# Performance work log

Hardware: AMD Instinct MI355X
Metric: run time of the kernel (lower is better)

Reference implementation:

```python
import jax, jax.numpy as jnp
import numpy as np

N = 50000; E = 800000; H = 4; C = 64; FEAT = 128; EDIM = 16; G = 256
NEG_SLOPE = 0.2; BN_EPS = 1e-5


def _gat_layer(x, src, dst, W, a_src, a_dst, bias, gamma, beta, alpha_edge=None):
    # GATConv (concat=True, PyG math), then BatchNorm1d (batch stats) + ReLU.
    h = (x @ W).reshape(N, H, C)                       # [N,H,C]
    alpha = (h * a_src).sum(-1)[src] + (h * a_dst).sum(-1)[dst]   # [Etot,H]
    if alpha_edge is not None:
        alpha = alpha + alpha_edge
    alpha = jax.nn.leaky_relu(alpha, NEG_SLOPE)
    amax = jax.ops.segment_max(alpha, dst, num_segments=N)        # edge softmax over dst
    ea = jnp.exp(alpha - amax[dst])
    denom = jax.ops.segment_sum(ea, dst, num_segments=N)
    coef = ea / (denom[dst] + 1e-16)
    out = jax.ops.segment_sum(coef[:, :, None] * h[src], dst, num_segments=N)
    out = out.reshape(N, H * C) + bias
    mu = out.mean(0)
    var = out.var(0)
    out = (out - mu) / jnp.sqrt(var + BN_EPS) * gamma + beta
    return jax.nn.relu(out)


def setup_inputs() -> dict:
    key = jax.random.key(0)
    ks = jax.random.split(key, 32)
    s = 0.05
    inp = {
        "x": jax.random.normal(ks[0], (N, FEAT), jnp.float32),
        "edge_index": jax.random.randint(ks[1], (2, E), 0, N),
        "edge_attr": jax.random.normal(ks[2], (E, EDIM), jnp.float32),
        "batch": jnp.sort(jax.random.randint(ks[3], (N,), 0, G)),
    }
    in_dims = [FEAT, H * C, H * C]
    for i in range(3):
        k = 4 + 7 * i
        inp[f"W{i}"] = jax.random.normal(ks[k], (in_dims[i], H * C), jnp.float32) * s
        inp[f"att_src{i}"] = jax.random.normal(ks[k + 1], (H, C), jnp.float32) * s
        inp[f"att_dst{i}"] = jax.random.normal(ks[k + 2], (H, C), jnp.float32) * s
        inp[f"bias{i}"] = jnp.zeros((H * C,), jnp.float32)
        inp[f"gamma{i}"] = jnp.ones((H * C,), jnp.float32)
        inp[f"beta{i}"] = jnp.zeros((H * C,), jnp.float32)
    inp["We0"] = jax.random.normal(ks[28], (EDIM, H * C), jnp.float32) * s
    inp["att_e0"] = jax.random.normal(ks[29], (H, C), jnp.float32) * s
    return inp


def reference(x, edge_index, edge_attr, batch,
              W0, att_src0, att_dst0, bias0, gamma0, beta0,
              W1, att_src1, att_dst1, bias1, gamma1, beta1,
              W2, att_src2, att_dst2, bias2, gamma2, beta2,
              We0, att_e0):
    # PyG GATConv adds self-loops; edge_attr for self-loops filled with mean.
    loops = jnp.arange(N)
    src = jnp.concatenate([edge_index[0], loops])
    dst = jnp.concatenate([edge_index[1], loops])
    ea_sl = jnp.concatenate([edge_attr, jnp.broadcast_to(edge_attr.mean(0), (N, EDIM))], 0)
    e = (ea_sl @ We0).reshape(E + N, H, C)
    alpha_e = (e * att_e0).sum(-1)                     # [Etot,H]
    x = _gat_layer(x, src, dst, W0, att_src0, att_dst0, bias0, gamma0, beta0, alpha_e)
    x = _gat_layer(x, src, dst, W1, att_src1, att_dst1, bias1, gamma1, beta1)
    x = _gat_layer(x, src, dst, W2, att_src2, att_dst2, bias2, gamma2, beta2)
    # global_mean_pool
    counts = jax.ops.segment_sum(jnp.ones((N,), x.dtype), batch, num_segments=G)
    sums = jax.ops.segment_sum(x, batch, num_segments=G)
    return sums / jnp.clip(counts, 1.0)[:, None]
```

## Files before the change

kernel.cpp:

```cpp
#include <hip/hip_runtime.h>
#include <math.h>

#define NN 50000
#define NE 800000
#define ET 850000
#define HCC 256
#define GG 256
#define CAP 64
#define NB 16

constexpr size_t NHC    = (size_t)NN * HCC;
constexpr size_t O_H    = 0;
constexpr size_t O_AGG  = O_H + NHC / 2;
constexpr size_t O_REC  = O_AGG + NHC / 2;
constexpr size_t O_BT0  = O_REC + (size_t)NN * CAP * 4;
constexpr size_t O_BT1  = O_BT0 + 16384;
constexpr size_t O_BT2  = O_BT1 + 32768;
constexpr size_t O_AS   = O_BT2 + 32768;
constexpr size_t O_AD   = O_AS + (size_t)NN * 4;
constexpr size_t O_M    = O_AD + (size_t)NN * 4;
constexpr size_t O_ZERO = O_M + 64;
constexpr size_t O_DEG  = O_ZERO;
constexpr size_t O_SLS  = O_DEG + NN;
constexpr size_t O_PART = O_SLS + 4;
constexpr size_t O_END  = O_PART + 3 * NB * 512;
constexpr size_t ZWORDS = O_END - O_ZERO;
constexpr int    ZBLK   = (int)((ZWORDS / 4 + 255) / 256);

typedef __attribute__((ext_vector_type(8))) short bf16x8;
typedef __attribute__((ext_vector_type(4))) float f32x4;

__device__ inline unsigned short f2bf(float f) {
    unsigned int u = __float_as_uint(f);
    unsigned int r = (u + 0x7fffu + ((u >> 16) & 1u)) >> 16;
    return (unsigned short)r;
}
__device__ inline float b2f(unsigned short u) {
    return __uint_as_float(((unsigned int)u) << 16);
}
__device__ inline float bflo(unsigned int u) { return __uint_as_float(u << 16); }
__device__ inline float bfhi(unsigned int u) { return __uint_as_float(u & 0xffff0000u); }

__global__ void prep_kernel(const float* __restrict__ W0, const float* __restrict__ W1,
                            const float* __restrict__ W2,
                            const float* __restrict__ We0, const float* __restrict__ att_e0,
                            unsigned short* __restrict__ Bt0,
                            unsigned short* __restrict__ Bt1,
                            unsigned short* __restrict__ Bt2,
                            float* __restrict__ M, float* __restrict__ zbase) {
    int b = blockIdx.x;
    if (b >= 641) {
        size_t idx = ((size_t)(b - 641) * 256 + threadIdx.x) * 4;
        if (idx < ZWORDS)
            *(float4*)(zbase + idx) = make_float4(0.f, 0.f, 0.f, 0.f);
        return;
    }
    if (b == 640) {
        int t = threadIdx.x;
        if (t < 64) {
            int k = t >> 2, hh = t & 3;
            float s = 0.f;
            for (int c = 0; c < 64; ++c)
                s += We0[k * 256 + hh * 64 + c] * att_e0[hh * 64 + c];
            M[k * 4 + hh] = s;
        }
        return;
    }
    const float* W; unsigned short* Bt; int K, base;
    if (b < 128)      { W = W0; Bt = Bt0; K = 128; base = 0; }
    else if (b < 384) { W = W1; Bt = Bt1; K = 256; base = 128; }
    else              { W = W2; Bt = Bt2; K = 256; base = 384; }
    int idx = (b - base) * 256 + threadIdx.x;
    int n = idx & 255, k = idx >> 8;
    Bt[(size_t)n * K + k] = f2bf(W[(size_t)k * 256 + n]);
}

__global__ void csr_kernel(const int* __restrict__ srcA, const int* __restrict__ dstA,
                           const float* __restrict__ ea, const float* __restrict__ M,
                           int* __restrict__ deg, uint4* __restrict__ rec,
                           float* __restrict__ slsum) {
    int t0 = blockIdx.x * 2048 + threadIdx.x;
    float a0 = 0.f, a1 = 0.f, a2 = 0.f, a3 = 0.f;
    #pragma unroll
    for (int q = 0; q < 8; ++q) {
        int e = t0 + q * 256;
        if (e < ET) {
            bool real = (e < NE);
            int d = real ? dstA[e] : (e - NE);
            int s = real ? srcA[e] : (e - NE);
            int p = atomicAdd(&deg[d], 1);
            if (p > CAP - 1) p = CAP - 1;
            int slot = d * CAP + p;
            uint4 r;
            r.z = (unsigned)s;
            if (real) {
                r.w = 0u;
                const float4* pp = (const float4*)(ea + (size_t)e * 16);
                float4 va = pp[0], vb = pp[1], vc = pp[2], vd = pp[3];
                float v[16] = {va.x, va.y, va.z, va.w, vb.x, vb.y, vb.z, vb.w,
                               vc.x, vc.y, vc.z, vc.w, vd.x, vd.y, vd.z, vd.w};
                float o0 = 0.f, o1 = 0.f, o2 = 0.f, o3 = 0.f;
                #pragma unroll
                for (int k = 0; k < 16; ++k) {
                    float4 m4 = *(const float4*)(M + k * 4);
                    o0 = fmaf(v[k], m4.x, o0);
                    o1 = fmaf(v[k], m4.y, o1);
                    o2 = fmaf(v[k], m4.z, o2);
                    o3 = fmaf(v[k], m4.w, o3);
                }
                r.x = ((unsigned)f2bf(o1) << 16) | (unsigned)f2bf(o0);
                r.y = ((unsigned)f2bf(o3) << 16) | (unsigned)f2bf(o2);
                a0 += o0; a1 += o1; a2 += o2; a3 += o3;
            } else {
                r.x = 0u; r.y = 0u; r.w = 1u;
            }
            rec[slot] = r;
        }
    }
    #pragma unroll
    for (int off = 32; off; off >>= 1) {
        a0 += __shfl_xor(a0, off);
        a1 += __shfl_xor(a1, off);
        a2 += __shfl_xor(a2, off);
        a3 += __shfl_xor(a3, off);
    }
    __shared__ float part[4][4];
    int wave = threadIdx.x >> 6, lane = threadIdx.x & 63;
    if (lane == 0) {
        part[wave][0] = a0; part[wave][1] = a1;
        part[wave][2] = a2; part[wave][3] = a3;
    }
    __syncthreads();
    if (threadIdx.x < 4)
        atomicAdd(&slsum[threadIdx.x],
                  part[0][threadIdx.x] + part[1][threadIdx.x] +
                  part[2][threadIdx.x] + part[3][threadIdx.x]);
}

template <int K, bool NORM>
__global__ __launch_bounds__(256) void gemm_fused(const float* __restrict__ Af,
                                                  const unsigned short* __restrict__ Ab,
                                                  const unsigned short* __restrict__ Bt,
                                                  const float* __restrict__ part,
                                                  const float* __restrict__ gamma,
                                                  const float* __restrict__ beta,
                                                  const float* __restrict__ att_src,
                                                  const float* __restrict__ att_dst,
                                                  unsigned short* __restrict__ Hout,
                                                  float* __restrict__ asA,
                                                  float* __restrict__ adA, int M) {
    __shared__ unsigned short As[64][40];
    __shared__ unsigned short Bs[256][40];
    __shared__ float kvs[256], cvs[256];
    int tid = threadIdx.x;
    int wave = tid >> 6, lane = tid & 63;
    int quad = lane >> 4, l16 = lane & 15;
    int row0 = blockIdx.x * 64;
    f32x4 acc[4][4] = {};

    if (NORM) {
        int ch = tid;
        float s = 0.f, s2 = 0.f;
        #pragma unroll
        for (int b = 0; b < NB; ++b) {
            s  += part[b * 512 + ch];
            s2 += part[b * 512 + 256 + ch];
        }
        const float invN = 1.0f / (float)NN;
        float mr = s * invN;
        float var = s2 * invN - mr * mr;
        float k = gamma[ch] * rsqrtf(var + 1e-5f);
        kvs[ch] = k;
        cvs[ch] = beta[ch] - mr * k;
        __syncthreads();
    }

    for (int k0 = 0; k0 < K; k0 += 32) {
        {
            int row = tid >> 2, seg = tid & 3;
            ushort4 o0 = make_ushort4(0, 0, 0, 0), o1 = o0;
            if (row0 + row < M) {
                float u[8];
                if (NORM) {
                    uint4 raw = *(const uint4*)(Ab + (size_t)(row0 + row) * K + k0 + seg * 8);
                    u[0] = bflo(raw.x); u[1] = bfhi(raw.x);
                    u[2] = bflo(raw.y); u[3] = bfhi(raw.y);
                    u[4] = bflo(raw.z); u[5] = bfhi(raw.z);
                    u[6] = bflo(raw.w); u[7] = bfhi(raw.w);
                    int cb = k0 + seg * 8;
                    #pragma unroll
                    for (int q = 0; q < 8; ++q)
                        u[q] = fmaxf(fmaf(u[q], kvs[cb + q], cvs[cb + q]), 0.f);
                } else {
                    const float* ap = Af + (size_t)(row0 + row) * K + k0 + seg * 8;
                    float4 f1 = *(const float4*)ap;
                    float4 f2 = *(const float4*)(ap + 4);
                    u[0] = f1.x; u[1] = f1.y; u[2] = f1.z; u[3] = f1.w;
                    u[4] = f2.x; u[5] = f2.y; u[6] = f2.z; u[7] = f2.w;
                }
                o0 = make_ushort4(f2bf(u[0]), f2bf(u[1]), f2bf(u[2]), f2bf(u[3]));
                o1 = make_ushort4(f2bf(u[4]), f2bf(u[5]), f2bf(u[6]), f2bf(u[7]));
            }
            *(ushort4*)&As[row][seg * 8] = o0;
            *(ushort4*)&As[row][seg * 8 + 4] = o1;
        }
        {
            const uint4* src = (const uint4*)(Bt + (size_t)tid * K + k0);
            uint4 b0 = src[0], b1 = src[1], b2 = src[2], b3 = src[3];
            uint4* dst = (uint4*)&Bs[tid][0];
            dst[0] = b0; dst[1] = b1; dst[2] = b2; dst[3] = b3;
        }
        __syncthreads();
        bf16x8 a_frag[4], b_frag[4];
        #pragma unroll
        for (int mi = 0; mi < 4; ++mi)
            a_frag[mi] = *(const bf16x8*)&As[mi * 16 + l16][quad * 8];
        #pragma unroll
        for (int ni = 0; ni < 4; ++ni)
            b_frag[ni] = *(const bf16x8*)&Bs[wave * 64 + ni * 16 + l16][quad * 8];
        #pragma unroll
        for (int mi = 0; mi < 4; ++mi)
            #pragma unroll
            for (int ni = 0; ni < 4; ++ni)
                acc[mi][ni] = __builtin_amdgcn_mfma_f32_16x16x32_bf16(
                    a_frag[mi], b_frag[ni], acc[mi][ni], 0, 0, 0);
        __syncthreads();
    }

    #pragma unroll
    for (int mi = 0; mi < 4; ++mi) {
        #pragma unroll
        for (int reg = 0; reg < 4; ++reg) {
            int r = row0 + mi * 16 + quad * 4 + reg;
            if (r < M) {
                #pragma unroll
                for (int ni = 0; ni < 4; ++ni) {
                    int c = wave * 64 + ni * 16 + l16;
                    Hout[(size_t)r * HCC + c] = f2bf(acc[mi][ni][reg]);
                }
            }
        }
    }
    float asc[4], adc_[4];
    #pragma unroll
    for (int ni = 0; ni < 4; ++ni) {
        asc[ni] = att_src[wave * 64 + ni * 16 + l16];
        adc_[ni] = att_dst[wave * 64 + ni * 16 + l16];
    }
    #pragma unroll
    for (int mi = 0; mi < 4; ++mi) {
        #pragma unroll
        for (int reg = 0; reg < 4; ++reg) {
            float s1 = acc[mi][0][reg] * asc[0] + acc[mi][1][reg] * asc[1] +
                       acc[mi][2][reg] * asc[2] + acc[mi][3][reg] * asc[3];
            float d1 = acc[mi][0][reg] * adc_[0] + acc[mi][1][reg] * adc_[1] +
                       acc[mi][2][reg] * adc_[2] + acc[mi][3][reg] * adc_[3];
            #pragma unroll
            for (int off = 1; off < 16; off <<= 1) {
                s1 += __shfl_xor(s1, off);
                d1 += __shfl_xor(d1, off);
            }
            int r = row0 + mi * 16 + quad * 4 + reg;
            if (l16 == 0 && r < M) {
                asA[(size_t)r * 4 + wave] = s1;
                adA[(size_t)r * 4 + wave] = d1;
            }
        }
    }
}

template <bool HAS_AE>
__global__ __launch_bounds__(512) void agg_kernel(const unsigned short* __restrict__ Hm,
                                                  const float* __restrict__ asA,
                                                  const float* __restrict__ adA,
                                                  const uint4* __restrict__ rec,
                                                  const int* __restrict__ degA,
                                                  const float* __restrict__ slsum,
                                                  unsigned short* __restrict__ outA,
                                                  float* __restrict__ part) {
    __shared__ float wlds[8][260];
    __shared__ float slds[2][8][256];
    int wave = threadIdx.x >> 6, lane = threadIdx.x & 63;
    int n = blockIdx.x * 8 + wave;
    int head = lane >> 4;
    int st = n * CAP;
    int d = degA[n];
    if (d > CAP) d = CAP;
    float4 ad4 = *(const float4*)(adA + (size_t)n * 4);

    float4 w4 = make_float4(0.f, 0.f, 0.f, 0.f);
    int ms = 0;
    if (lane < d) {
        uint4 r = rec[st + lane];
        ms = (int)r.z;
        float4 av = *(const float4*)(asA + (size_t)ms * 4);
        float4 t = make_float4(av.x + ad4.x, av.y + ad4.y, av.z + ad4.z, av.w + ad4.w);
        if (HAS_AE) {
            if (r.w) {
                const float inv = 1.0f / (float)NE;
                t.x += slsum[0] * inv; t.y += slsum[1] * inv;
                t.z += slsum[2] * inv; t.w += slsum[3] * inv;
            } else {
                t.x += bflo(r.x); t.y += bfhi(r.x);
                t.z += bflo(r.y); t.w += bfhi(r.y);
            }
        }
        t.x = (t.x > 0.f) ? t.x : 0.2f * t.x;
        t.y = (t.y > 0.f) ? t.y : 0.2f * t.y;
        t.z = (t.z > 0.f) ? t.z : 0.2f * t.z;
        t.w = (t.w > 0.f) ? t.w : 0.2f * t.w;
        w4.x = __expf(t.x);
        w4.y = __expf(t.y);
        w4.z = __expf(t.z);
        w4.w = __expf(t.w);
    }
    float4 Dv = w4;
    wlds[wave][0 * 65 + lane] = w4.x;
    wlds[wave][1 * 65 + lane] = w4.y;
    wlds[wave][2 * 65 + lane] = w4.z;
    wlds[wave][3 * 65 + lane] = w4.w;

    float4 acc = make_float4(0.f, 0.f, 0.f, 0.f);
    const unsigned short* hb = Hm + lane * 4;
    int cnt8 = (d + 7) & ~7;
    const float* wrow = &wlds[wave][head * 65];

    int sjA[8]; ushort4 hvA[8];
    #pragma unroll
    for (int q = 0; q < 8; ++q)
        sjA[q] = __builtin_amdgcn_readlane(ms, q);
    #pragma unroll
    for (int q = 0; q < 8; ++q)
        hvA[q] = *(const ushort4*)(hb + (size_t)sjA[q] * HCC);
    for (int jj = 0; jj < cnt8; jj += 8) {
        int nj = jj + 8;
        bool more = (nj < cnt8);
        ushort4 hvB[8];
        if (more) {
            int sjB[8];
            #pragma unroll
            for (int q = 0; q < 8; ++q)
                sjB[q] = __builtin_amdgcn_readlane(ms, nj + q);
            #pragma unroll
            for (int q = 0; q < 8; ++q)
                hvB[q] = *(const ushort4*)(hb + (size_t)sjB[q] * HCC);
        }
        float wq[8];
        #pragma unroll
        for (int q = 0; q < 8; ++q)
            wq[q] = wrow[jj + q];
        #pragma unroll
        for (int q = 0; q < 8; ++q) {
            acc.x = fmaf(wq[q], b2f(hvA[q].x), acc.x);
            acc.y = fmaf(wq[q], b2f(hvA[q].y), acc.y);
            acc.z = fmaf(wq[q], b2f(hvA[q].z), acc.z);
            acc.w = fmaf(wq[q], b2f(hvA[q].w), acc.w);
        }
        if (more) {
            #pragma unroll
            for (int q = 0; q < 8; ++q)
                hvA[q] = hvB[q];
        }
    }
    #pragma unroll
    for (int off = 32; off; off >>= 1) {
        Dv.x += __shfl_xor(Dv.x, off);
        Dv.y += __shfl_xor(Dv.y, off);
        Dv.z += __shfl_xor(Dv.z, off);
        Dv.w += __shfl_xor(Dv.w, off);
    }
    float D = (head & 2) ? ((head & 1) ? Dv.w : Dv.z) : ((head & 1) ? Dv.y : Dv.x);
    float inv = 1.0f / (D + 1e-16f);
    float4 o = make_float4(acc.x * inv, acc.y * inv, acc.z * inv, acc.w * inv);
    ushort4 ob = make_ushort4(f2bf(o.x), f2bf(o.y), f2bf(o.z), f2bf(o.w));
    *(ushort4*)(outA + (size_t)n * HCC + lane * 4) = ob;

    *(float4*)&slds[0][wave][lane * 4] = o;
    *(float4*)&slds[1][wave][lane * 4] =
        make_float4(o.x * o.x, o.y * o.y, o.z * o.z, o.w * o.w);
    __syncthreads();
    int t = threadIdx.x;
    if (t < 512) {
        int ch = t & 255, which = t >> 8;
        float s = 0.f;
        #pragma unroll
        for (int w = 0; w < 8; ++w)
            s += slds[which][w][ch];
        int bucket = blockIdx.x & (NB - 1);
        atomicAdd(&part[bucket * 512 + which * 256 + ch], s);
    }
}

__global__ void pool_kernel(const unsigned short* __restrict__ aggb,
                            const float* __restrict__ part,
                            const float* __restrict__ gamma, const float* __restrict__ beta,
                            const int* __restrict__ batch,
                            float* __restrict__ out) {
    int ch = threadIdx.x;
    int g = blockIdx.x;
    float s = 0.f, s2 = 0.f;
    #pragma unroll
    for (int b = 0; b < NB; ++b) {
        s  += part[b * 512 + ch];
        s2 += part[b * 512 + 256 + ch];
    }
    const float invN = 1.0f / (float)NN;
    float mr = s * invN;
    float var = s2 * invN - mr * mr;
    float k = gamma[ch] * rsqrtf(var + 1e-5f);
    float c = beta[ch] - mr * k;

    int lo = 0, hi = NN;
    while (lo < hi) { int mid = (lo + hi) >> 1; if (batch[mid] < g) lo = mid + 1; else hi = mid; }
    int start = lo;
    lo = start; hi = NN;
    while (lo < hi) { int mid = (lo + hi) >> 1; if (batch[mid] < g + 1) lo = mid + 1; else hi = mid; }
    int end = lo;

    float a0 = 0.f, a1 = 0.f, a2 = 0.f, a3 = 0.f;
    int n = start;
    for (; n + 3 < end; n += 4) {
        a0 += fmaxf(fmaf(b2f(aggb[(size_t)n * HCC + ch]), k, c), 0.f);
        a1 += fmaxf(fmaf(b2f(aggb[(size_t)(n + 1) * HCC + ch]), k, c), 0.f);
        a2 += fmaxf(fmaf(b2f(aggb[(size_t)(n + 2) * HCC + ch]), k, c), 0.f);
        a3 += fmaxf(fmaf(b2f(aggb[(size_t)(n + 3) * HCC + ch]), k, c), 0.f);
    }
    for (; n < end; ++n)
        a0 += fmaxf(fmaf(b2f(aggb[(size_t)n * HCC + ch]), k, c), 0.f);
    float tot = (a0 + a1) + (a2 + a3);
    out[(size_t)g * HCC + ch] = tot / fmaxf((float)(end - start), 1.0f);
}

extern "C" void kernel_launch(void* const* d_in, const int* in_sizes, int n_in,
                              void* d_out, int out_size, void* d_ws, size_t ws_size,
                              hipStream_t stream) {
    const float* x = (const float*)d_in[0];
    const int* edge_index = (const int*)d_in[1];
    const int* srcA = edge_index;
    const int* dstA = edge_index + NE;
    const float* edge_attr = (const float*)d_in[2];
    const int* batch = (const int*)d_in[3];
    const float* W[3]   = {(const float*)d_in[4],  (const float*)d_in[10], (const float*)d_in[16]};
    const float* asc[3] = {(const float*)d_in[5],  (const float*)d_in[11], (const float*)d_in[17]};
    const float* adc[3] = {(const float*)d_in[6],  (const float*)d_in[12], (const float*)d_in[18]};
    const float* gam[3] = {(const float*)d_in[8],  (const float*)d_in[14], (const float*)d_in[20]};
    const float* bet[3] = {(const float*)d_in[9],  (const float*)d_in[15], (const float*)d_in[21]};
    const float* We0 = (const float*)d_in[22];
    const float* att_e0 = (const float*)d_in[23];

    float* wsf = (float*)d_ws;
    unsigned short* hbuf = (unsigned short*)(wsf + O_H);
    unsigned short* aggb = (unsigned short*)(wsf + O_AGG);
    uint4* rec   = (uint4*)(wsf + O_REC);
    unsigned short* Bt0  = (unsigned short*)(wsf + O_BT0);
    unsigned short* Bt1  = (unsigned short*)(wsf + O_BT1);
    unsigned short* Bt2  = (unsigned short*)(wsf + O_BT2);
    float* asA   = wsf + O_AS;
    float* adA   = wsf + O_AD;
    float* Mb    = wsf + O_M;
    int*   deg   = (int*)(wsf + O_DEG);
    float* slsum = wsf + O_SLS;
    float* part  = wsf + O_PART;

    prep_kernel<<<641 + ZBLK, 256, 0, stream>>>(W[0], W[1], W[2], We0, att_e0,
                                                Bt0, Bt1, Bt2, Mb, wsf + O_ZERO);
    csr_kernel<<<(ET + 2047) / 2048, 256, 0, stream>>>(srcA, dstA, edge_attr, Mb,
                                                       deg, rec, slsum);

    unsigned short* Bts[3] = {Bt0, Bt1, Bt2};
    for (int L = 0; L < 3; ++L) {
        if (L == 0)
            gemm_fused<128, false><<<782, 256, 0, stream>>>(x, (const unsigned short*)0,
                Bts[0], (const float*)0, gam[0], bet[0], asc[0], adc[0], hbuf, asA, adA, NN);
        else
            gemm_fused<256, true><<<782, 256, 0, stream>>>((const float*)0, aggb,
                Bts[L], part + (size_t)(L - 1) * NB * 512, gam[L - 1], bet[L - 1],
                asc[L], adc[L], hbuf, asA, adA, NN);
        if (L == 0)
            agg_kernel<true><<<6250, 512, 0, stream>>>(hbuf, asA, adA, rec, deg, slsum,
                aggb, part + (size_t)L * NB * 512);
        else
            agg_kernel<false><<<6250, 512, 0, stream>>>(hbuf, asA, adA, rec, deg, slsum,
                aggb, part + (size_t)L * NB * 512);
    }

    pool_kernel<<<GG, 256, 0, stream>>>(aggb, part + (size_t)2 * NB * 512,
                                        gam[2], bet[2], batch, (float*)d_out);
}
```

Baseline: 528.5 us.

## Make GEMM persistent with resident B half-tile and double-buffered A prefetch

Replaces the per-tile GEMM with a persistent kernel. Each block keeps a 128-column slice of the bf16 weight matrix resident in LDS for the full K, then loops over 64-row tiles, prefetching the next A tile into registers while computing on the current one in a double-buffered LDS array. The fp32 input x is now converted to bf16 in the prep kernel, so layer 0 also reads bf16. This is meant to avoid reloading B for every tile and to hide global A-load latency, at the cost of much larger LDS use (lower occupancy) and fewer blocks.

```diff
diff --git a/kernel.cpp b/kernel.cpp
--- a/kernel.cpp
+++ b/kernel.cpp
@@ -8,6 +8,8 @@
 #define GG 256
 #define CAP 64
 #define NB 16
+
+constexpr int RTILES = 782;
 
 constexpr size_t NHC    = (size_t)NN * HCC;
 constexpr size_t O_H    = 0;
@@ -26,6 +28,7 @@
 constexpr size_t O_END  = O_PART + 3 * NB * 512;
 constexpr size_t ZWORDS = O_END - O_ZERO;
 constexpr int    ZBLK   = (int)((ZWORDS / 4 + 255) / 256);
+constexpr int    XBLK   = (int)((size_t)NN * 128 / 2048);
 
 typedef __attribute__((ext_vector_type(8))) short bf16x8;
 typedef __attribute__((ext_vector_type(4))) float f32x4;
@@ -47,8 +50,21 @@
                             unsigned short* __restrict__ Bt0,
                             unsigned short* __restrict__ Bt1,
                             unsigned short* __restrict__ Bt2,
-                            float* __restrict__ M, float* __restrict__ zbase) {
+                            float* __restrict__ M, float* __restrict__ zbase,
+                            const float* __restrict__ x, unsigned short* __restrict__ xb) {
     int b = blockIdx.x;
+    if (b >= 641 + ZBLK) {
+        size_t i0 = ((size_t)(b - (641 + ZBLK)) * 256 + threadIdx.x) * 8;
+        float4 f1 = *(const float4*)(x + i0);
+        float4 f2 = *(const float4*)(x + i0 + 4);
+        uint4 o;
+        o.x = ((unsigned)f2bf(f1.y) << 16) | f2bf(f1.x);
+        o.y = ((unsigned)f2bf(f1.w) << 16) | f2bf(f1.z);
+        o.z = ((unsigned)f2bf(f2.y) << 16) | f2bf(f2.x);
+        o.w = ((unsigned)f2bf(f2.w) << 16) | f2bf(f2.z);
+        *(uint4*)(xb + i0) = o;
+        return;
+    }
     if (b >= 641) {
         size_t idx = ((size_t)(b - 641) * 256 + threadIdx.x) * 4;
         if (idx < ZWORDS)
@@ -138,33 +154,41 @@
 }
 
 template <int K, bool NORM>
-__global__ __launch_bounds__(256) void gemm_fused(const float* __restrict__ Af,
-                                                  const unsigned short* __restrict__ Ab,
-                                                  const unsigned short* __restrict__ Bt,
-                                                  const float* __restrict__ part,
-                                                  const float* __restrict__ gamma,
-                                                  const float* __restrict__ beta,
-                                                  const float* __restrict__ att_src,
-                                                  const float* __restrict__ att_dst,
-                                                  unsigned short* __restrict__ Hout,
-                                                  float* __restrict__ asA,
-                                                  float* __restrict__ adA, int M) {
-    __shared__ unsigned short As[64][40];
-    __shared__ unsigned short Bs[256][40];
+__global__ __launch_bounds__(256) void gemm2(const unsigned short* __restrict__ Ab,
+                                             const unsigned short* __restrict__ Bt,
+                                             const float* __restrict__ part,
+                                             const float* __restrict__ gamma,
+                                             const float* __restrict__ beta,
+                                             const float* __restrict__ att_src,
+                                             const float* __restrict__ att_dst,
+                                             unsigned short* __restrict__ Hout,
+                                             float* __restrict__ asA,
+                                             float* __restrict__ adA, int M) {
+    constexpr int KP  = K + 8;
+    constexpr int NLD = K / 32;
+    __shared__ unsigned short Bs[128][KP];
+    __shared__ unsigned short As[2][64][KP];
     __shared__ float kvs[256], cvs[256];
+
     int tid = threadIdx.x;
     int wave = tid >> 6, lane = tid & 63;
     int quad = lane >> 4, l16 = lane & 15;
-    int row0 = blockIdx.x * 64;
-    f32x4 acc[4][4] = {};
+    int wr = wave & 1, wc = wave >> 1;
+
+    int b = blockIdx.x;
+    int cb = (b >> 3) & 1;
+    int ts = ((b >> 4) << 3) | (b & 7);
+    int np = (int)(gridDim.x >> 1);
+    int colbase = cb * 128;
+    int head = cb * 2 + wc;
 
     if (NORM) {
         int ch = tid;
         float s = 0.f, s2 = 0.f;
         #pragma unroll
-        for (int b = 0; b < NB; ++b) {
-            s  += part[b * 512 + ch];
-            s2 += part[b * 512 + 256 + ch];
+        for (int q = 0; q < NB; ++q) {
+            s  += part[q * 512 + ch];
+            s2 += part[q * 512 + 256 + ch];
         }
         const float invN = 1.0f / (float)NN;
         float mr = s * invN;
@@ -172,100 +196,123 @@
         float k = gamma[ch] * rsqrtf(var + 1e-5f);
         kvs[ch] = k;
         cvs[ch] = beta[ch] - mr * k;
+    }
+    {
+        constexpr int TOT = 128 * K;
+        for (int idx = tid * 8; idx < TOT; idx += 2048) {
+            int br = idx / K, bk = idx % K;
+            uint4 v = *(const uint4*)(Bt + (size_t)(colbase + br) * K + bk);
+            *(uint4*)&Bs[br][bk] = v;
+        }
+    }
+
+    int srow = tid >> 2;
+    const int scol0 = (tid & 3) * (K / 4);
+
+    uint4 ldA_[NLD], ldB_[NLD];
+
+    auto issue = [&](uint4 (&ld)[NLD], int t) {
+        int r = t * 64 + srow;
+        if (r < M) {
+            const uint4* src = (const uint4*)(Ab + (size_t)r * K + scol0);
+            #pragma unroll
+            for (int q = 0; q < NLD; ++q) ld[q] = src[q];
+        } else {
+            #pragma unroll
+            for (int q = 0; q < NLD; ++q) ld[q] = make_uint4(0u, 0u, 0u, 0u);
+        }
+    };
+    auto commit = [&](uint4 (&ld)[NLD], int buf) {
+        #pragma unroll
+        for (int q = 0; q < NLD; ++q) {
+            uint4 v = ld[q];
+            if (NORM) {
+                int ch = scol0 + q * 8;
+                float u[8] = {bflo(v.x), bfhi(v.x), bflo(v.y), bfhi(v.y),
+                              bflo(v.z), bfhi(v.z), bflo(v.w), bfhi(v.w)};
+                #pragma unroll
+                for (int j = 0; j < 8; ++j)
+                    u[j] = fmaxf(fmaf(u[j], kvs[ch + j], cvs[ch + j]), 0.f);
+                v.x = ((unsigned)f2bf(u[1]) << 16) | f2bf(u[0]);
+                v.y = ((unsigned)f2bf(u[3]) << 16) | f2bf(u[2]);
+                v.z = ((unsigned)f2bf(u[5]) << 16) | f2bf(u[4]);
+                v.w = ((unsigned)f2bf(u[7]) << 16) | f2bf(u[6]);
+            }
+            *(uint4*)&As[buf][srow][scol0 + q * 8] = v;
+        }
+    };
+
+    float asc[4], adc_[4];
+    #pragma unroll
+    for (int ni = 0; ni < 4; ++ni) {
+        int c = colbase + wc * 64 + ni * 16 + l16;
+        asc[ni]  = att_src[c];
+        adc_[ni] = att_dst[c];
+    }
+
+    __syncthreads();
+
+    auto tilestep = [&](uint4 (&ldCur)[NLD], uint4 (&ldNxt)[NLD], int buf, int t, int tn) {
+        if (tn < RTILES) issue(ldNxt, tn);
+        commit(ldCur, buf);
         __syncthreads();
-    }
-
-    for (int k0 = 0; k0 < K; k0 += 32) {
-        {
-            int row = tid >> 2, seg = tid & 3;
-            ushort4 o0 = make_ushort4(0, 0, 0, 0), o1 = o0;
-            if (row0 + row < M) {
-                float u[8];
-                if (NORM) {
-                    uint4 raw = *(const uint4*)(Ab + (size_t)(row0 + row) * K + k0 + seg * 8);
-                    u[0] = bflo(raw.x); u[1] = bfhi(raw.x);
-                    u[2] = bflo(raw.y); u[3] = bfhi(raw.y);
-                    u[4] = bflo(raw.z); u[5] = bfhi(raw.z);
-                    u[6] = bflo(raw.w); u[7] = bfhi(raw.w);
-                    int cb = k0 + seg * 8;
+        f32x4 acc[2][4] = {};
+        #pragma unroll
+        for (int k0 = 0; k0 < K; k0 += 32) {
+            bf16x8 af[2], bfr[4];
+            #pragma unroll
+            for (int mi = 0; mi < 2; ++mi)
+                af[mi] = *(const bf16x8*)&As[buf][wr * 32 + mi * 16 + l16][k0 + quad * 8];
+            #pragma unroll
+            for (int ni = 0; ni < 4; ++ni)
+                bfr[ni] = *(const bf16x8*)&Bs[wc * 64 + ni * 16 + l16][k0 + quad * 8];
+            #pragma unroll
+            for (int mi = 0; mi < 2; ++mi)
+                #pragma unroll
+                for (int ni = 0; ni < 4; ++ni)
+                    acc[mi][ni] = __builtin_amdgcn_mfma_f32_16x16x32_bf16(
+                        af[mi], bfr[ni], acc[mi][ni], 0, 0, 0);
+        }
+        int row0 = t * 64 + wr * 32;
+        #pragma unroll
+        for (int mi = 0; mi < 2; ++mi) {
+            #pragma unroll
+            for (int reg = 0; reg < 4; ++reg) {
+                int r = row0 + mi * 16 + quad * 4 + reg;
+                if (r < M) {
                     #pragma unroll
-                    for (int q = 0; q < 8; ++q)
-                        u[q] = fmaxf(fmaf(u[q], kvs[cb + q], cvs[cb + q]), 0.f);
-                } else {
-                    const float* ap = Af + (size_t)(row0 + row) * K + k0 + seg * 8;
-                    float4 f1 = *(const float4*)ap;
-                    float4 f2 = *(const float4*)(ap + 4);
-                    u[0] = f1.x; u[1] = f1.y; u[2] = f1.z; u[3] = f1.w;
-                    u[4] = f2.x; u[5] = f2.y; u[6] = f2.z; u[7] = f2.w;
+                    for (int ni = 0; ni < 4; ++ni) {
+                        int c = colbase + wc * 64 + ni * 16 + l16;
+                        Hout[(size_t)r * HCC + c] = f2bf(acc[mi][ni][reg]);
+                    }
                 }
-                o0 = make_ushort4(f2bf(u[0]), f2bf(u[1]), f2bf(u[2]), f2bf(u[3]));
-                o1 = make_ushort4(f2bf(u[4]), f2bf(u[5]), f2bf(u[6]), f2bf(u[7]));
-            }
-            *(ushort4*)&As[row][seg * 8] = o0;
-            *(ushort4*)&As[row][seg * 8 + 4] = o1;
-        }
-        {
-            const uint4* src = (const uint4*)(Bt + (size_t)tid * K + k0);
-            uint4 b0 = src[0], b1 = src[1], b2 = src[2], b3 = src[3];
-            uint4* dst = (uint4*)&Bs[tid][0];
-            dst[0] = b0; dst[1] = b1; dst[2] = b2; dst[3] = b3;
-        }
-        __syncthreads();
-        bf16x8 a_frag[4], b_frag[4];
-        #pragma unroll
-        for (int mi = 0; mi < 4; ++mi)
-            a_frag[mi] = *(const bf16x8*)&As[mi * 16 + l16][quad * 8];
-        #pragma unroll
-        for (int ni = 0; ni < 4; ++ni)
-            b_frag[ni] = *(const bf16x8*)&Bs[wave * 64 + ni * 16 + l16][quad * 8];
-        #pragma unroll
-        for (int mi = 0; mi < 4; ++mi)
-            #pragma unroll
-            for (int ni = 0; ni < 4; ++ni)
-                acc[mi][ni] = __builtin_amdgcn_mfma_f32_16x16x32_bf16(
-                    a_frag[mi], b_frag[ni], acc[mi][ni], 0, 0, 0);
-        __syncthreads();
-    }
-
-    #pragma unroll
-    for (int mi = 0; mi < 4; ++mi) {
-        #pragma unroll
-        for (int reg = 0; reg < 4; ++reg) {
-            int r = row0 + mi * 16 + quad * 4 + reg;
-            if (r < M) {
+                float s1 = acc[mi][0][reg] * asc[0] + acc[mi][1][reg] * asc[1] +
+                           acc[mi][2][reg] * asc[2] + acc[mi][3][reg] * asc[3];
+                float d1 = acc[mi][0][reg] * adc_[0] + acc[mi][1][reg] * adc_[1] +
+                           acc[mi][2][reg] * adc_[2] + acc[mi][3][reg] * adc_[3];
                 #pragma unroll
-                for (int ni = 0; ni < 4; ++ni) {
-                    int c = wave * 64 + ni * 16 + l16;
-                    Hout[(size_t)r * HCC + c] = f2bf(acc[mi][ni][reg]);
+                for (int off = 1; off < 16; off <<= 1) {
+                    s1 += __shfl_xor(s1, off);
+                    d1 += __shfl_xor(d1, off);
+                }
+                if (l16 == 0 && r < M) {
+                    asA[(size_t)r * 4 + head] = s1;
+                    adA[(size_t)r * 4 + head] = d1;
                 }
             }
         }
-    }
-    float asc[4], adc_[4];
-    #pragma unroll
-    for (int ni = 0; ni < 4; ++ni) {
-        asc[ni] = att_src[wave * 64 + ni * 16 + l16];
-        adc_[ni] = att_dst[wave * 64 + ni * 16 + l16];
-    }
-    #pragma unroll
-    for (int mi = 0; mi < 4; ++mi) {
-        #pragma unroll
-        for (int reg = 0; reg < 4; ++reg) {
-            float s1 = acc[mi][0][reg] * asc[0] + acc[mi][1][reg] * asc[1] +
-                       acc[mi][2][reg] * asc[2] + acc[mi][3][reg] * asc[3];
-            float d1 = acc[mi][0][reg] * adc_[0] + acc[mi][1][reg] * adc_[1] +
-                       acc[mi][2][reg] * adc_[2] + acc[mi][3][reg] * adc_[3];
-            #pragma unroll
-            for (int off = 1; off < 16; off <<= 1) {
-                s1 += __shfl_xor(s1, off);
-                d1 += __shfl_xor(d1, off);
-            }
-            int r = row0 + mi * 16 + quad * 4 + reg;
-            if (l16 == 0 && r < M) {
-                asA[(size_t)r * 4 + wave] = s1;
-                adA[(size_t)r * 4 + wave] = d1;
-            }
-        }
+    };
+
+    int t = ts;
+    issue(ldA_, t);
+    while (t < RTILES) {
+        int t1 = t + np;
+        tilestep(ldA_, ldB_, 0, t, t1);
+        t = t1;
+        if (t >= RTILES) break;
+        int t2 = t + np;
+        tilestep(ldB_, ldA_, 1, t, t2);
+        t = t2;
     }
 }
 
@@ -451,6 +498,7 @@
     float* wsf = (float*)d_ws;
     unsigned short* hbuf = (unsigned short*)(wsf + O_H);
     unsigned short* aggb = (unsigned short*)(wsf + O_AGG);
+    unsigned short* xb   = aggb;
     uint4* rec   = (uint4*)(wsf + O_REC);
     unsigned short* Bt0  = (unsigned short*)(wsf + O_BT0);
     unsigned short* Bt1  = (unsigned short*)(wsf + O_BT1);
@@ -462,27 +510,26 @@
     float* slsum = wsf + O_SLS;
     float* part  = wsf + O_PART;
 
-    prep_kernel<<<641 + ZBLK, 256, 0, stream>>>(W[0], W[1], W[2], We0, att_e0,
-                                                Bt0, Bt1, Bt2, Mb, wsf + O_ZERO);
+    prep_kernel<<<641 + ZBLK + XBLK, 256, 0, stream>>>(W[0], W[1], W[2], We0, att_e0,
+                                                       Bt0, Bt1, Bt2, Mb, wsf + O_ZERO,
+                                                       x, xb);
     csr_kernel<<<(ET + 2047) / 2048, 256, 0, stream>>>(srcA, dstA, edge_attr, Mb,
                                                        deg, rec, slsum);
 
-    unsigned short* Bts[3] = {Bt0, Bt1, Bt2};
-    for (int L = 0; L < 3; ++L) {
-        if (L == 0)
-            gemm_fused<128, false><<<782, 256, 0, stream>>>(x, (const unsigned short*)0,
-                Bts[0], (const float*)0, gam[0], bet[0], asc[0], adc[0], hbuf, asA, adA, NN);
-        else
-            gemm_fused<256, true><<<782, 256, 0, stream>>>((const float*)0, aggb,
-                Bts[L], part + (size_t)(L - 1) * NB * 512, gam[L - 1], bet[L - 1],
-                asc[L], adc[L], hbuf, asA, adA, NN);
-        if (L == 0)
-            agg_kernel<true><<<6250, 512, 0, stream>>>(hbuf, asA, adA, rec, deg, slsum,
-                aggb, part + (size_t)L * NB * 512);
-        else
-            agg_kernel<false><<<6250, 512, 0, stream>>>(hbuf, asA, adA, rec, deg, slsum,
-                aggb, part + (size_t)L * NB * 512);
-    }
+    gemm2<128, false><<<512, 256, 0, stream>>>(xb, Bt0, (const float*)0,
+        (const float*)0, (const float*)0, asc[0], adc[0], hbuf, asA, adA, NN);
+    agg_kernel<true><<<6250, 512, 0, stream>>>(hbuf, asA, adA, rec, deg, slsum,
+        aggb, part + (size_t)0 * NB * 512);
+
+    gemm2<256, true><<<256, 256, 0, stream>>>(aggb, Bt1, part + (size_t)0 * NB * 512,
+        gam[0], bet[0], asc[1], adc[1], hbuf, asA, adA, NN);
+    agg_kernel<false><<<6250, 512, 0, stream>>>(hbuf, asA, adA, rec, deg, slsum,
+        aggb, part + (size_t)1 * NB * 512);
+
+    gemm2<256, true><<<256, 256, 0, stream>>>(aggb, Bt2, part + (size_t)1 * NB * 512,
+        gam[1], bet[1], asc[2], adc[2], hbuf, asA, adA, NN);
+    agg_kernel<false><<<6250, 512, 0, stream>>>(hbuf, asA, adA, rec, deg, slsum,
+        aggb, part + (size_t)2 * NB * 512);
 
     pool_kernel<<<GG, 256, 0, stream>>>(aggb, part + (size_t)2 * NB * 512,
                                         gam[2], bet[2], batch, (float*)d_out);
```

After: 535.8 us. No clear change (+1.4%).
